# Kernel optimization log

Hardware: AMD Instinct MI355X
Metric: run time of the kernel (lower is better)

## Reference

```python
import jax, jax.numpy as jnp
import numpy as np

DIM = 128
HEADS = 8
DIM_HEAD = 128  # must equal DIM for the module's shapes to be consistent
INNER = HEADS * DIM_HEAD  # 1024
B, N = 16, 2048
SCALE = 1.0 / (DIM // 2 + 1)  # 1/65


def setup_inputs() -> dict:
    key = jax.random.key(0)
    k1, k2, k3 = jax.random.split(key, 3)
    x = jax.random.normal(k1, (B, N, DIM), dtype=jnp.float32)
    w_qkv = jax.random.normal(k2, (DIM, 3 * INNER), dtype=jnp.float32) * (DIM ** -0.5)
    w_out = jax.random.normal(k3, (INNER, DIM), dtype=jnp.float32) * (INNER ** -0.5)
    b_out = jnp.zeros((DIM,), dtype=jnp.float32)
    return {"x": x, "w_qkv": w_qkv, "w_out": w_out, "b_out": b_out}


def reference(x, w_qkv, w_out, b_out):
    b, n, dim = x.shape
    qkv = x @ w_qkv                                   # [b, n, 3*inner]
    q, k, v = jnp.split(qkv, 3, axis=-1)
    # b n (h d) -> b h n d
    to_heads = lambda t: t.reshape(b, n, HEADS, DIM_HEAD).transpose(0, 2, 1, 3)
    q, k, v = to_heads(q), to_heads(k), to_heads(v)
    xq_ft = jnp.abs(jnp.fft.rfft(q * SCALE, axis=-1))  # [b, h, n, f] real
    xk_ft = jnp.abs(jnp.fft.rfft(k * SCALE, axis=-1))
    xv_ft = jnp.fft.rfft(v, axis=-1)                   # complex
    att = jnp.einsum('bhex,bhey->bhxy', xq_ft, xk_ft)  # [b, h, f, f]
    att = jax.nn.softmax(att, axis=-1)
    xqkv_ft = jnp.einsum('bhxy,bhey->bhex', att.astype(xv_ft.dtype), xv_ft)
    out = jnp.fft.irfft(xqkv_ft, n=dim, axis=-1)       # [b, h, n, dim]
    out = out.transpose(0, 2, 1, 3).reshape(b, n, HEADS * dim)  # b n (h d)
    return out @ w_out + b_out
```

## Files before the change

### kernel.cpp

```cpp
#include <hip/hip_runtime.h>
#include <hip/hip_bf16.h>
#include <math.h>

#define NB    16
#define NSEQ  2048
#define MROWS (NB*NSEQ)

typedef __attribute__((ext_vector_type(8))) short bf16x8;
typedef __attribute__((ext_vector_type(4))) float f32x4;

__device__ __forceinline__ void g2l16(const void* g, void* l) {
    __builtin_amdgcn_global_load_lds(
        (const __attribute__((address_space(1))) void*)g,
        (__attribute__((address_space(3))) void*)l, 16, 0, 0);
}

__device__ __forceinline__ ushort f2bfu(float x) {
    __hip_bfloat16 t = __float2bfloat16(x);
    return *reinterpret_cast<ushort*>(&t);
}

__global__ __launch_bounds__(256) void k_misc(const float* __restrict__ x,
                                              const float* __restrict__ wqkv,
                                              const float* __restrict__ wout,
                                              __hip_bfloat16* __restrict__ Xb,
                                              ushort* __restrict__ Wvb,
                                              ushort* __restrict__ Wqkb,
                                              ushort* __restrict__ Gcat,
                                              ushort* __restrict__ Fcs,
                                              ushort* __restrict__ Bas) {
    __shared__ float tc[128], ts[128];
    int tid = threadIdx.x;
    int bid = blockIdx.x;
    if (bid < 4096) {
        int i = bid * 256 + tid;
        float4 v = ((const float4*)x)[i];
        __hip_bfloat16 o[4] = {__float2bfloat16(v.x), __float2bfloat16(v.y),
                               __float2bfloat16(v.z), __float2bfloat16(v.w)};
        *(ushort4*)((ushort*)Xb + (size_t)i * 4) = *(const ushort4*)o;
    } else if (bid < 4224) {
        int u = bid - 4096;
        float4 v = *(const float4*)(wqkv + (size_t)u * 3072 + 2048 + tid * 4);
        ushort o[4] = {f2bfu(v.x), f2bfu(v.y), f2bfu(v.z), f2bfu(v.w)};
        *(ushort4*)(Wvb + (size_t)u * 1024 + tid * 4) = *(const ushort4*)o;
    } else if (bid < 4352) {
        int u = bid - 4224;
        #pragma unroll
        for (int it = 0; it < 2; ++it) {
            int i = it * 256 + tid;
            float4 v = ((const float4*)(wqkv + (size_t)u * 3072))[i];
            ushort o[4] = {f2bfu(v.x), f2bfu(v.y), f2bfu(v.z), f2bfu(v.w)};
            *(ushort4*)(Wqkb + (size_t)u * 2048 + i * 4) = *(const ushort4*)o;
        }
    } else if (bid < 4872) {
        int hx = bid - 4352;
        if (tid < 128) {
            float a = (float)tid / 64.0f;
            tc[tid] = cospif(a);
            ts[tid] = sinpif(a);
        }
        __syncthreads();
        if (tid < 128) {
            int h = hx / 65, xx = hx - h * 65;
            float w = (xx == 0 || xx == 64) ? (1.0f / 128.0f) : (2.0f / 128.0f);
            float ar = 0.f, ai = 0.f;
            #pragma unroll 8
            for (int d = 0; d < 128; ++d) {
                float wv = wout[(size_t)(h * 128 + d) * 128 + tid];
                int m = (xx * d) & 127;
                ar = fmaf(wv, tc[m], ar);
                ai = fmaf(wv, ts[m], ai);
            }
            ushort* gp = Gcat + ((size_t)(h * 128 + tid)) * 160;
            gp[xx] = f2bfu(ar * w);
            gp[80 + xx] = f2bfu(-ai * w);
            if (xx == 0) {
                for (int k = 65; k < 80; ++k) gp[k] = 0;
                for (int k = 145; k < 160; ++k) gp[k] = 0;
            }
        }
    } else if (bid < 4888) {
        int r = (bid - 4872) * 16 + (tid >> 4);
        int d = r & 127;
        int y0 = (tid & 15) * 6;
        #pragma unroll
        for (int k = 0; k < 6; ++k) {
            int y = y0 + k;
            float v = 0.f;
            if (y < 65) {
                float a = (float)((d * y) & 127) / 64.0f;
                v = (r < 128) ? cospif(a) : -sinpif(a);
            }
            Fcs[r * 96 + y] = f2bfu(v);
        }
    } else {
        int idx = bid - 4888;
        int rj = idx * 16 + (tid >> 4);
        int ri = (rj >= 80) ? 1 : 0;
        int f = rj - ri * 80;
        int d0 = (tid & 15) * 8;
        #pragma unroll
        for (int k = 0; k < 8; ++k) {
            int d = d0 + k;
            float a = (float)((f * d) & 127) / 64.0f;
            float v = (ri ? -sinpif(a) : cospif(a)) * (1.0f / 65.0f);
            Bas[rj * 128 + d] = f2bfu(v);
        }
    }
}

__global__ __launch_bounds__(256) void k_wfold(const ushort* __restrict__ Wqkb,
                                               const ushort* __restrict__ Bas,
                                               ushort* __restrict__ Wt2) {
    __shared__ ushort As[64 * 128];
    __shared__ ushort Bs[160 * 128];
    int tid = threadIdx.x;
    int wave = tid >> 6, lane = tid & 63;
    int reg = blockIdx.x >> 4;
    int h = (blockIdx.x >> 1) & 7;
    int uh = blockIdx.x & 1;
    const ushort* ga = Wqkb + (size_t)(uh * 64) * 2048 + reg * 1024 + h * 128;
    #pragma unroll
    for (int it = 0; it < 4; ++it) {
        int q0 = wave * 256 + it * 64;
        int q = q0 + lane;
        int row = q >> 4, cp = q & 15;
        int gc = cp ^ (row & 15);
        g2l16(ga + (size_t)row * 2048 + gc * 8, As + q0 * 8);
    }
    #pragma unroll
    for (int it = 0; it < 10; ++it) {
        int q0 = it * 256 + wave * 64;
        int q = q0 + lane;
        int row = q >> 4, cp = q & 15;
        int gc = cp ^ (row & 15);
        g2l16(Bas + (size_t)row * 128 + gc * 8, Bs + q0 * 8);
    }
    __syncthreads();

    f32x4 acc[2][5];
    #pragma unroll
    for (int i = 0; i < 2; ++i)
        #pragma unroll
        for (int j = 0; j < 5; ++j) acc[i][j] = (f32x4){0.f, 0.f, 0.f, 0.f};

    int lr = lane & 15, lk = lane >> 4;
    int wr = (wave >> 1) * 32;
    int wn = (wave & 1) * 80;
    #pragma unroll
    for (int kk = 0; kk < 4; ++kk) {
        bf16x8 af[2], bfr[5];
        int c = kk * 4 + lk;
        #pragma unroll
        for (int i = 0; i < 2; ++i) {
            int m = wr + i * 16 + lr;
            af[i] = *(const bf16x8*)(As + m * 128 + (c ^ (m & 15)) * 8);
        }
        #pragma unroll
        for (int j = 0; j < 5; ++j) {
            int n = wn + j * 16 + lr;
            bfr[j] = *(const bf16x8*)(Bs + n * 128 + (c ^ (n & 15)) * 8);
        }
        #pragma unroll
        for (int i = 0; i < 2; ++i)
            #pragma unroll
            for (int j = 0; j < 5; ++j)
                acc[i][j] = __builtin_amdgcn_mfma_f32_16x16x32_bf16(af[i], bfr[j], acc[i][j], 0, 0, 0);
    }

    #pragma unroll
    for (int j = 0; j < 5; ++j) {
        int rj = wn + j * 16 + lr;
        int n = (h * 2 + reg) * 160 + rj;
        #pragma unroll
        for (int i = 0; i < 2; ++i) {
            int c0 = uh * 64 + wr + i * 16 + lk * 4;
            union { ushort4 u4; ushort u[4]; } pk;
            #pragma unroll
            for (int r = 0; r < 4; ++r) pk.u[r] = f2bfu(acc[i][j][r]);
            *(ushort4*)(Wt2 + (size_t)n * 128 + c0) = pk.u4;
        }
    }
}

__global__ __launch_bounds__(320, 3) void k_fuse(const __hip_bfloat16* __restrict__ Xb,
                                                 const ushort* __restrict__ Wt2,
                                                 float* __restrict__ attp) {
    __shared__ ushort As[128 * 128];
    __shared__ ushort S[160 * 128];
    int tid = threadIdx.x;
    int wave = tid >> 6, lane = tid & 63;
    int lr = lane & 15, lk = lane >> 4;
    int lin = blockIdx.y * 128 + blockIdx.x;
    int nl = (lin & 7) * 64 + (lin >> 3);
    int b = nl >> 5;
    int epart = (nl >> 3) & 3, h = nl & 7;
    size_t erow0 = (size_t)b * NSEQ + (size_t)epart * 512;
    const ushort* wh = Wt2 + (size_t)h * 320 * 128;

    bf16x8 bw[4][4];
    #pragma unroll
    for (int ks = 0; ks < 4; ++ks)
        #pragma unroll
        for (int rb = 0; rb < 4; ++rb) {
            int n = rb * 80 + wave * 16 + lr;
            bw[ks][rb] = *(const bf16x8*)(wh + (size_t)n * 128 + (ks * 4 + lk) * 8);
        }

    {
        const ushort* gx = (const ushort*)Xb + erow0 * 128;
        for (int r = wave; r < 32; r += 5) {
            int q0 = r * 64, q = q0 + lane;
            int row = q >> 4, cp = q & 15;
            int gc = cp ^ (row & 15);
            g2l16(gx + (size_t)row * 128 + gc * 8, As + q0 * 8);
        }
    }
    __syncthreads();

    f32x4 acc2[5];
    #pragma unroll
    for (int j = 0; j < 5; ++j) acc2[j] = (f32x4){0.f, 0.f, 0.f, 0.f};

    for (int it = 0; it < 4; ++it) {
        #pragma unroll
        for (int et = 0; et < 8; ++et) {
            f32x4 a4[4];
            #pragma unroll
            for (int rb = 0; rb < 4; ++rb) a4[rb] = (f32x4){0.f, 0.f, 0.f, 0.f};
            #pragma unroll
            for (int ks = 0; ks < 4; ++ks) {
                int m = et * 16 + lr;
                bf16x8 xa = *(const bf16x8*)(As + m * 128 + (((ks * 4 + lk) ^ (m & 15))) * 8);
                #pragma unroll
                for (int rb = 0; rb < 4; ++rb)
                    a4[rb] = __builtin_amdgcn_mfma_f32_16x16x32_bf16(xa, bw[ks][rb], a4[rb], 0, 0, 0);
            }
            int e4 = et * 16 + lk * 4;
            int cq = e4 >> 3, sub = e4 & 7;
            union { ushort4 u4; ushort u[4]; } pq, pk2;
            #pragma unroll
            for (int r = 0; r < 4; ++r) {
                pq.u[r]  = f2bfu(__builtin_amdgcn_sqrtf(a4[0][r] * a4[0][r] + a4[1][r] * a4[1][r]));
                pk2.u[r] = f2bfu(__builtin_amdgcn_sqrtf(a4[2][r] * a4[2][r] + a4[3][r] * a4[3][r]));
            }
            int fq = wave * 16 + lr;
            int fk = 80 + wave * 16 + lr;
            *(ushort4*)(S + fq * 128 + ((cq ^ (fq & 15)) << 3) + sub) = pq.u4;
            *(ushort4*)(S + fk * 128 + ((cq ^ (fk & 15)) << 3) + sub) = pk2.u4;
        }
        __syncthreads();
        if (it < 3) {
            const ushort* gx = (const ushort*)Xb + (erow0 + (size_t)(it + 1) * 128) * 128;
            for (int r = wave; r < 32; r += 5) {
                int q0 = r * 64, q = q0 + lane;
                int row = q >> 4, cp = q & 15;
                int gc = cp ^ (row & 15);
                g2l16(gx + (size_t)row * 128 + gc * 8, As + q0 * 8);
            }
        }
        #pragma unroll
        for (int ks = 0; ks < 4; ++ks) {
            int cg = ks * 4 + lk;
            int xr = wave * 16 + lr;
            bf16x8 qa = *(const bf16x8*)(S + xr * 128 + ((cg ^ (xr & 15)) << 3));
            #pragma unroll
            for (int kt = 0; kt < 5; ++kt) {
                int yr = 80 + kt * 16 + lr;
                bf16x8 kb = *(const bf16x8*)(S + yr * 128 + ((cg ^ (yr & 15)) << 3));
                acc2[kt] = __builtin_amdgcn_mfma_f32_16x16x32_bf16(qa, kb, acc2[kt], 0, 0, 0);
            }
        }
        __syncthreads();
    }

    float* outp = attp + ((size_t)(b * 8 + h) * 4 + epart) * 6400;
    #pragma unroll
    for (int kt = 0; kt < 5; ++kt)
        #pragma unroll
        for (int r = 0; r < 4; ++r)
            outp[(wave * 16 + lk * 4 + r) * 80 + kt * 16 + lr] = acc2[kt][r];
}

__global__ __launch_bounds__(256) void k_TP(const float* __restrict__ attp,
                                            const ushort* __restrict__ Fcs,
                                            const ushort* __restrict__ Gcat,
                                            ushort* __restrict__ Pt) {
    __shared__ ushort A3[128 * 168];
    __shared__ ushort Ab[80 * 104];
    int tid = threadIdx.x;
    int wave = tid >> 6, lane = tid & 63;
    int lr = lane & 15, quad = lane >> 4;
    int bh = blockIdx.x, chalf = blockIdx.y;
    int b = bh >> 3, h = bh & 7;

    uint2 z2; z2.x = 0; z2.y = 0;
    uint2* A3v = (uint2*)A3;
    #pragma unroll 4
    for (int i = tid; i < 128 * 168 / 4; i += 256) A3v[i] = z2;
    uint2* Abv = (uint2*)Ab;
    #pragma unroll 4
    for (int i = tid; i < 80 * 104 / 4; i += 256) Abv[i] = z2;
    __syncthreads();

    const float* pbase = attp + (size_t)bh * 4 * 6400;
    for (int p = 0; p < 17; ++p) {
        int xx = p * 4 + wave;
        if (xx < 65) {
            float v0 = 0.f, v1 = 0.f;
            #pragma unroll
            for (int c = 0; c < 4; ++c) {
                v0 += pbase[(size_t)c * 6400 + xx * 80 + lane];
                if (lane == 0) v1 += pbase[(size_t)c * 6400 + xx * 80 + 64];
            }
            float v1b = __shfl(v1, 0);
            float m = fmaxf(v0, v1b);
            #pragma unroll
            for (int off = 32; off >= 1; off >>= 1) m = fmaxf(m, __shfl_xor(m, off));
            float e0 = expf(v0 - m);
            float e1 = expf(v1b - m);
            float s = e0;
            #pragma unroll
            for (int off = 32; off >= 1; off >>= 1) s += __shfl_xor(s, off);
            s += e1;
            float inv = 1.0f / s;
            Ab[xx * 104 + lane] = f2bfu(e0 * inv);
            if (lane == 0) Ab[xx * 104 + 64] = f2bfu(e1 * inv);
        }
    }
    __syncthreads();

    f32x4 acc1[4][5];
    #pragma unroll
    for (int i = 0; i < 4; ++i)
        #pragma unroll
        for (int j = 0; j < 5; ++j) acc1[i][j] = (f32x4){0.f, 0.f, 0.f, 0.f};
    #pragma unroll
    for (int ks = 0; ks < 3; ++ks) {
        bf16x8 af[4], bfr[5];
        #pragma unroll
        for (int mi = 0; mi < 4; ++mi)
            af[mi] = *(const bf16x8*)(Fcs + (size_t)((wave * 4 + mi) * 16 + lr) * 96 + ks * 32 + quad * 8);
        #pragma unroll
        for (int nt = 0; nt < 5; ++nt)
            bfr[nt] = *(const bf16x8*)(Ab + (nt * 16 + lr) * 104 + ks * 32 + quad * 8);
        #pragma unroll
        for (int mi = 0; mi < 4; ++mi)
            #pragma unroll
            for (int nt = 0; nt < 5; ++nt)
                acc1[mi][nt] = __builtin_amdgcn_mfma_f32_16x16x32_bf16(af[mi], bfr[nt], acc1[mi][nt], 0, 0, 0);
    }
    #pragma unroll
    for (int nt = 0; nt < 5; ++nt) {
        int x = nt * 16 + lr;
        if (x < 65) {
            #pragma unroll
            for (int mi = 0; mi < 4; ++mi) {
                int wbase = (wave * 4 + mi) * 16 + quad * 4;
                #pragma unroll
                for (int r = 0; r < 4; ++r) {
                    int which = wbase + r;
                    int d = which & 127;
                    int kc = (which >> 7) * 80 + x;
                    A3[d * 168 + kc] = f2bfu(acc1[mi][nt][r]);
                }
            }
        }
    }
    __syncthreads();

    f32x4 acc2[2][4];
    #pragma unroll
    for (int i = 0; i < 2; ++i)
        #pragma unroll
        for (int j = 0; j < 4; ++j) acc2[i][j] = (f32x4){0.f, 0.f, 0.f, 0.f};
    const ushort* Gh = Gcat + (size_t)h * 128 * 160;
    #pragma unroll
    for (int ks = 0; ks < 5; ++ks) {
        bf16x8 a2[2], b2[4];
        #pragma unroll
        for (int mi = 0; mi < 2; ++mi)
            a2[mi] = *(const bf16x8*)(A3 + ((wave * 2 + mi) * 16 + lr) * 168 + ks * 32 + quad * 8);
        #pragma unroll
        for (int nt = 0; nt < 4; ++nt)
            b2[nt] = *(const bf16x8*)(Gh + (size_t)(chalf * 64 + nt * 16 + lr) * 160 + ks * 32 + quad * 8);
        #pragma unroll
        for (int mi = 0; mi < 2; ++mi)
            #pragma unroll
            for (int nt = 0; nt < 4; ++nt)
                acc2[mi][nt] = __builtin_amdgcn_mfma_f32_16x16x32_bf16(a2[mi], b2[nt], acc2[mi][nt], 0, 0, 0);
    }
    #pragma unroll
    for (int mi = 0; mi < 2; ++mi) {
        int dbase = (wave * 2 + mi) * 16 + quad * 4;
        #pragma unroll
        for (int nt = 0; nt < 4; ++nt) {
            int c = chalf * 64 + nt * 16 + lr;
            union { ushort4 u4; ushort u[4]; } pk;
            #pragma unroll
            for (int r = 0; r < 4; ++r) pk.u[r] = f2bfu(acc2[mi][nt][r]);
            *(ushort4*)(Pt + ((size_t)(b * 128 + c)) * 1024 + h * 128 + dbase) = pk.u4;
        }
    }
}

__global__ __launch_bounds__(256) void k_R(const ushort* __restrict__ Wvb,
                                           const ushort* __restrict__ Pt,
                                           ushort* __restrict__ Rt) {
    __shared__ ushort As[64 * 128];
    __shared__ ushort Bs[64 * 128];
    int tid = threadIdx.x;
    int wave = tid >> 6, lane = tid & 63;
    int b = blockIdx.x >> 2;
    int nq = (blockIdx.x >> 1) & 1;
    int uq = blockIdx.x & 1;
    const ushort* pb = Pt + (size_t)b * 128 * 1024;

    f32x4 acc[2][2];
    #pragma unroll
    for (int i = 0; i < 2; ++i)
        #pragma unroll
        for (int j = 0; j < 2; ++j) acc[i][j] = (f32x4){0.f, 0.f, 0.f, 0.f};

    int lr = lane & 15, lk = lane >> 4;
    int wr = (wave >> 1) * 32, wc = (wave & 1) * 32;

    for (int k0 = 0; k0 < 1024; k0 += 128) {
        __syncthreads();
        #pragma unroll
        for (int it = 0; it < 4; ++it) {
            int q = wave * 256 + it * 64 + lane;
            int row = q >> 4, cp = q & 15;
            int gc = cp ^ (row & 15);
            int lbase = (wave * 256 + it * 64) * 8;
            g2l16(Wvb + (size_t)(uq * 64 + row) * 1024 + k0 + gc * 8, As + lbase);
            g2l16(pb + (size_t)(nq * 64 + row) * 1024 + k0 + gc * 8, Bs + lbase);
        }
        __syncthreads();
        #pragma unroll
        for (int kk = 0; kk < 4; ++kk) {
            bf16x8 af[2], bfr[2];
            int c = kk * 4 + lk;
            #pragma unroll
            for (int i = 0; i < 2; ++i) {
                int m = wr + i * 16 + lr;
                af[i] = *(const bf16x8*)(As + m * 128 + (c ^ (m & 15)) * 8);
                int n = wc + i * 16 + lr;
                bfr[i] = *(const bf16x8*)(Bs + n * 128 + (c ^ (n & 15)) * 8);
            }
            #pragma unroll
            for (int i = 0; i < 2; ++i)
                #pragma unroll
                for (int j = 0; j < 2; ++j)
                    acc[i][j] = __builtin_amdgcn_mfma_f32_16x16x32_bf16(af[i], bfr[j], acc[i][j], 0, 0, 0);
        }
    }
    #pragma unroll
    for (int i = 0; i < 2; ++i) {
        int ubase = uq * 64 + wr + i * 16 + lk * 4;
        #pragma unroll
        for (int j = 0; j < 2; ++j) {
            int n = nq * 64 + wc + j * 16 + lr;
            union { ushort4 u4; ushort u[4]; } pk;
            #pragma unroll
            for (int r = 0; r < 4; ++r) pk.u[r] = f2bfu(acc[i][j][r]);
            *(ushort4*)(Rt + (size_t)b * 16384 + n * 128 + ubase) = pk.u4;
        }
    }
}

__global__ __launch_bounds__(256) void k_out(const __hip_bfloat16* __restrict__ Xb,
                                             const ushort* __restrict__ Rt,
                                             const float* __restrict__ bout,
                                             float* __restrict__ out) {
    __shared__ ushort As[128 * 128];
    __shared__ ushort Bs[128 * 128];
    int tid = threadIdx.x;
    int wave = tid >> 6, lane = tid & 63;
    int m0 = blockIdx.x * 128;
    int b = blockIdx.x >> 4;
    const ushort* ga = (const ushort*)Xb + (size_t)m0 * 128;
    const ushort* gb = Rt + (size_t)b * 16384;
    #pragma unroll
    for (int it = 0; it < 8; ++it) {
        int q = wave * 512 + it * 64 + lane;
        int row = q >> 4, cp = q & 15;
        int gc = cp ^ (row & 15);
        int lbase = (wave * 512 + it * 64) * 8;
        g2l16(ga + (size_t)row * 128 + gc * 8, As + lbase);
        g2l16(gb + (size_t)row * 128 + gc * 8, Bs + lbase);
    }
    __syncthreads();

    f32x4 acc[4][4];
    #pragma unroll
    for (int i = 0; i < 4; ++i)
        #pragma unroll
        for (int j = 0; j < 4; ++j) acc[i][j] = (f32x4){0.f, 0.f, 0.f, 0.f};

    int lr = lane & 15, lk = lane >> 4;
    int wr = (wave >> 1) * 64, wc = (wave & 1) * 64;
    #pragma unroll
    for (int kk = 0; kk < 4; ++kk) {
        bf16x8 af[4], bfr[4];
        int c = kk * 4 + lk;
        #pragma unroll
        for (int i = 0; i < 4; ++i) {
            int m = wr + i * 16 + lr;
            af[i] = *(const bf16x8*)(As + m * 128 + (c ^ (m & 15)) * 8);
            int n = wc + i * 16 + lr;
            bfr[i] = *(const bf16x8*)(Bs + n * 128 + (c ^ (n & 15)) * 8);
        }
        #pragma unroll
        for (int i = 0; i < 4; ++i)
            #pragma unroll
            for (int j = 0; j < 4; ++j)
                acc[i][j] = __builtin_amdgcn_mfma_f32_16x16x32_bf16(af[i], bfr[j], acc[i][j], 0, 0, 0);
    }

    #pragma unroll
    for (int i = 0; i < 4; ++i) {
        int gr = m0 + wr + i * 16 + lk * 4;
        #pragma unroll
        for (int j = 0; j < 4; ++j) {
            int gcol = wc + j * 16 + lr;
            float bias = bout[gcol];
            #pragma unroll
            for (int r = 0; r < 4; ++r)
                out[(size_t)(gr + r) * 128 + gcol] = acc[i][j][r] + bias;
        }
    }
}

extern "C" void kernel_launch(void* const* d_in, const int* in_sizes, int n_in,
                              void* d_out, int out_size, void* d_ws, size_t ws_size,
                              hipStream_t stream) {
    const float* x    = (const float*)d_in[0];
    const float* wqkv = (const float*)d_in[1];
    const float* wout = (const float*)d_in[2];
    const float* bout = (const float*)d_in[3];
    float* out = (float*)d_out;

    char* ws = (char*)d_ws;
    size_t off = 0;
    auto alloc = [&](size_t bytes) -> void* {
        void* p = (void*)(ws + off);
        off += (bytes + 255) & ~(size_t)255;
        return p;
    };
    ushort* Wt2  = (ushort*)alloc((size_t)8 * 320 * 128 * 2);
    ushort* Gcat = (ushort*)alloc((size_t)8 * 128 * 160 * 2);
    ushort* Fcs  = (ushort*)alloc((size_t)256 * 96 * 2);
    ushort* Wvb  = (ushort*)alloc((size_t)128 * 1024 * 2);
    ushort* Wqkb = (ushort*)alloc((size_t)128 * 2048 * 2);
    ushort* Bas  = (ushort*)alloc((size_t)160 * 128 * 2);
    __hip_bfloat16* Xb = (__hip_bfloat16*)alloc((size_t)MROWS * 128 * 2);
    float* attp = (float*)alloc((size_t)128 * 4 * 6400 * 4);
    ushort* Pt  = (ushort*)alloc((size_t)16 * 128 * 1024 * 2);
    ushort* Rt  = (ushort*)alloc((size_t)16 * 128 * 128 * 2);

    k_misc<<<dim3(4898), 256, 0, stream>>>(x, wqkv, wout, Xb, Wvb, Wqkb, Gcat, Fcs, Bas);
    k_wfold<<<dim3(32), 256, 0, stream>>>(Wqkb, Bas, Wt2);
    k_fuse<<<dim3(128, 4), 320, 0, stream>>>(Xb, Wt2, attp);
    k_TP<<<dim3(128, 2), 256, 0, stream>>>(attp, Fcs, Gcat, Pt);
    k_R<<<dim3(64), 256, 0, stream>>>(Wvb, Pt, Rt);
    k_out<<<dim3(256), 256, 0, stream>>>(Xb, Rt, bout, out);
}
```

Measured before the change: 168.1 us.

## Halve k_fuse tiles for higher occupancy and split softmax into its own kernel

k_fuse now processes 256-row sequence chunks with 64-row tiles instead of 512/128. It streams Wt2 fragments per half instead of holding all of them in registers, and the launch-bounds occupancy hint rises from 3 to 5 blocks. This cuts LDS and register use and doubles the grid to raise occupancy. The softmax that k_TP used to compute redundantly in each of its two blocks per head now runs once in a separate kernel that writes bf16 attention. That adds a launch and doubles the partial-sum traffic, and the Wt2 loads now repeat every iteration.

Measured after the change: 183.1 us. 1.09x slower.

```diff
diff --git a/kernel.cpp b/kernel.cpp
--- a/kernel.cpp
+++ b/kernel.cpp
@@ -183,33 +183,25 @@
     }
 }
 
-__global__ __launch_bounds__(320, 3) void k_fuse(const __hip_bfloat16* __restrict__ Xb,
+__global__ __launch_bounds__(320, 5) void k_fuse(const __hip_bfloat16* __restrict__ Xb,
                                                  const ushort* __restrict__ Wt2,
                                                  float* __restrict__ attp) {
-    __shared__ ushort As[128 * 128];
-    __shared__ ushort S[160 * 128];
+    __shared__ ushort As[64 * 128];
+    __shared__ ushort S[160 * 64];
     int tid = threadIdx.x;
     int wave = tid >> 6, lane = tid & 63;
     int lr = lane & 15, lk = lane >> 4;
     int lin = blockIdx.y * 128 + blockIdx.x;
-    int nl = (lin & 7) * 64 + (lin >> 3);
-    int b = nl >> 5;
-    int epart = (nl >> 3) & 3, h = nl & 7;
-    size_t erow0 = (size_t)b * NSEQ + (size_t)epart * 512;
+    int nl = (lin & 7) * 128 + (lin >> 3);
+    int b = nl >> 6;
+    int rem = nl & 63;
+    int h = rem >> 3, epart = rem & 7;
+    size_t erow0 = (size_t)b * NSEQ + (size_t)epart * 256;
     const ushort* wh = Wt2 + (size_t)h * 320 * 128;
-
-    bf16x8 bw[4][4];
-    #pragma unroll
-    for (int ks = 0; ks < 4; ++ks)
-        #pragma unroll
-        for (int rb = 0; rb < 4; ++rb) {
-            int n = rb * 80 + wave * 16 + lr;
-            bw[ks][rb] = *(const bf16x8*)(wh + (size_t)n * 128 + (ks * 4 + lk) * 8);
-        }
 
     {
         const ushort* gx = (const ushort*)Xb + erow0 * 128;
-        for (int r = wave; r < 32; r += 5) {
+        for (int r = wave; r < 16; r += 5) {
             int q0 = r * 64, q = q0 + lane;
             int row = q >> 4, cp = q & 15;
             int gc = cp ^ (row & 15);
@@ -224,35 +216,41 @@
 
     for (int it = 0; it < 4; ++it) {
         #pragma unroll
-        for (int et = 0; et < 8; ++et) {
-            f32x4 a4[4];
-            #pragma unroll
-            for (int rb = 0; rb < 4; ++rb) a4[rb] = (f32x4){0.f, 0.f, 0.f, 0.f};
-            #pragma unroll
-            for (int ks = 0; ks < 4; ++ks) {
-                int m = et * 16 + lr;
-                bf16x8 xa = *(const bf16x8*)(As + m * 128 + (((ks * 4 + lk) ^ (m & 15))) * 8);
+        for (int p = 0; p < 2; ++p) {
+            bf16x8 bwp[4][2];
+            #pragma unroll
+            for (int ks = 0; ks < 4; ++ks)
                 #pragma unroll
-                for (int rb = 0; rb < 4; ++rb)
-                    a4[rb] = __builtin_amdgcn_mfma_f32_16x16x32_bf16(xa, bw[ks][rb], a4[rb], 0, 0, 0);
-            }
-            int e4 = et * 16 + lk * 4;
-            int cq = e4 >> 3, sub = e4 & 7;
-            union { ushort4 u4; ushort u[4]; } pq, pk2;
-            #pragma unroll
-            for (int r = 0; r < 4; ++r) {
-                pq.u[r]  = f2bfu(__builtin_amdgcn_sqrtf(a4[0][r] * a4[0][r] + a4[1][r] * a4[1][r]));
-                pk2.u[r] = f2bfu(__builtin_amdgcn_sqrtf(a4[2][r] * a4[2][r] + a4[3][r] * a4[3][r]));
-            }
-            int fq = wave * 16 + lr;
-            int fk = 80 + wave * 16 + lr;
-            *(ushort4*)(S + fq * 128 + ((cq ^ (fq & 15)) << 3) + sub) = pq.u4;
-            *(ushort4*)(S + fk * 128 + ((cq ^ (fk & 15)) << 3) + sub) = pk2.u4;
+                for (int j = 0; j < 2; ++j) {
+                    int n = (p * 2 + j) * 80 + wave * 16 + lr;
+                    bwp[ks][j] = *(const bf16x8*)(wh + (size_t)n * 128 + (ks * 4 + lk) * 8);
+                }
+            #pragma unroll
+            for (int et = 0; et < 4; ++et) {
+                f32x4 a2[2];
+                a2[0] = (f32x4){0.f, 0.f, 0.f, 0.f};
+                a2[1] = (f32x4){0.f, 0.f, 0.f, 0.f};
+                #pragma unroll
+                for (int ks = 0; ks < 4; ++ks) {
+                    int m = et * 16 + lr;
+                    bf16x8 xa = *(const bf16x8*)(As + m * 128 + (((ks * 4 + lk) ^ (m & 15))) * 8);
+                    a2[0] = __builtin_amdgcn_mfma_f32_16x16x32_bf16(xa, bwp[ks][0], a2[0], 0, 0, 0);
+                    a2[1] = __builtin_amdgcn_mfma_f32_16x16x32_bf16(xa, bwp[ks][1], a2[1], 0, 0, 0);
+                }
+                int e4 = et * 16 + lk * 4;
+                int cq = e4 >> 3, sub = e4 & 7;
+                union { ushort4 u4; ushort u[4]; } pm;
+                #pragma unroll
+                for (int r = 0; r < 4; ++r)
+                    pm.u[r] = f2bfu(__builtin_amdgcn_sqrtf(a2[0][r] * a2[0][r] + a2[1][r] * a2[1][r]));
+                int f = p * 80 + wave * 16 + lr;
+                *(ushort4*)(S + f * 64 + ((cq ^ (f & 7)) << 3) + sub) = pm.u4;
+            }
         }
         __syncthreads();
         if (it < 3) {
-            const ushort* gx = (const ushort*)Xb + (erow0 + (size_t)(it + 1) * 128) * 128;
-            for (int r = wave; r < 32; r += 5) {
+            const ushort* gx = (const ushort*)Xb + (erow0 + (size_t)(it + 1) * 64) * 128;
+            for (int r = wave; r < 16; r += 5) {
                 int q0 = r * 64, q = q0 + lane;
                 int row = q >> 4, cp = q & 15;
                 int gc = cp ^ (row & 15);
@@ -260,21 +258,21 @@
             }
         }
         #pragma unroll
-        for (int ks = 0; ks < 4; ++ks) {
-            int cg = ks * 4 + lk;
+        for (int ksq = 0; ksq < 2; ++ksq) {
+            int cg = ksq * 4 + lk;
             int xr = wave * 16 + lr;
-            bf16x8 qa = *(const bf16x8*)(S + xr * 128 + ((cg ^ (xr & 15)) << 3));
+            bf16x8 qa = *(const bf16x8*)(S + xr * 64 + ((cg ^ (xr & 7)) << 3));
             #pragma unroll
             for (int kt = 0; kt < 5; ++kt) {
                 int yr = 80 + kt * 16 + lr;
-                bf16x8 kb = *(const bf16x8*)(S + yr * 128 + ((cg ^ (yr & 15)) << 3));
+                bf16x8 kb = *(const bf16x8*)(S + yr * 64 + ((cg ^ (yr & 7)) << 3));
                 acc2[kt] = __builtin_amdgcn_mfma_f32_16x16x32_bf16(qa, kb, acc2[kt], 0, 0, 0);
             }
         }
         __syncthreads();
     }
 
-    float* outp = attp + ((size_t)(b * 8 + h) * 4 + epart) * 6400;
+    float* outp = attp + ((size_t)(b * 8 + h) * 8 + epart) * 6400;
     #pragma unroll
     for (int kt = 0; kt < 5; ++kt)
         #pragma unroll
@@ -282,53 +280,56 @@
             outp[(wave * 16 + lk * 4 + r) * 80 + kt * 16 + lr] = acc2[kt][r];
 }
 
-__global__ __launch_bounds__(256) void k_TP(const float* __restrict__ attp,
+__global__ void k_softmax(const float* __restrict__ attp, ushort* __restrict__ AttB) {
+    int xx = blockIdx.x;
+    int bh = blockIdx.y;
+    int lane = threadIdx.x;
+    ushort* Ab = AttB + (size_t)bh * 8320;
+    if (xx >= 65) {
+        Ab[xx * 104 + lane] = 0;
+        if (lane < 40) Ab[xx * 104 + 64 + lane] = 0;
+        return;
+    }
+    const float* base = attp + (size_t)bh * 8 * 6400 + xx * 80;
+    float v0 = 0.f, v1 = 0.f;
+    #pragma unroll
+    for (int c = 0; c < 8; ++c) {
+        v0 += base[(size_t)c * 6400 + lane];
+        if (lane == 0) v1 += base[(size_t)c * 6400 + 64];
+    }
+    float v1b = __shfl(v1, 0);
+    float m = fmaxf(v0, v1b);
+    #pragma unroll
+    for (int off = 32; off >= 1; off >>= 1) m = fmaxf(m, __shfl_xor(m, off));
+    float e0 = expf(v0 - m);
+    float e1 = expf(v1b - m);
+    float s = e0;
+    #pragma unroll
+    for (int off = 32; off >= 1; off >>= 1) s += __shfl_xor(s, off);
+    s += e1;
+    float inv = 1.0f / s;
+    Ab[xx * 104 + lane] = f2bfu(e0 * inv);
+    if (lane == 0) Ab[xx * 104 + 64] = f2bfu(e1 * inv);
+    if (lane < 39) Ab[xx * 104 + 65 + lane] = 0;
+}
+
+__global__ __launch_bounds__(256) void k_TP(const ushort* __restrict__ AttB,
                                             const ushort* __restrict__ Fcs,
                                             const ushort* __restrict__ Gcat,
                                             ushort* __restrict__ Pt) {
     __shared__ ushort A3[128 * 168];
-    __shared__ ushort Ab[80 * 104];
     int tid = threadIdx.x;
     int wave = tid >> 6, lane = tid & 63;
     int lr = lane & 15, quad = lane >> 4;
-    int bh = blockIdx.x, chalf = blockIdx.y;
+    int chalf = blockIdx.x, bh = blockIdx.y;
     int b = bh >> 3, h = bh & 7;
 
     uint2 z2; z2.x = 0; z2.y = 0;
     uint2* A3v = (uint2*)A3;
     #pragma unroll 4
     for (int i = tid; i < 128 * 168 / 4; i += 256) A3v[i] = z2;
-    uint2* Abv = (uint2*)Ab;
-    #pragma unroll 4
-    for (int i = tid; i < 80 * 104 / 4; i += 256) Abv[i] = z2;
     __syncthreads();
-
-    const float* pbase = attp + (size_t)bh * 4 * 6400;
-    for (int p = 0; p < 17; ++p) {
-        int xx = p * 4 + wave;
-        if (xx < 65) {
-            float v0 = 0.f, v1 = 0.f;
-            #pragma unroll
-            for (int c = 0; c < 4; ++c) {
-                v0 += pbase[(size_t)c * 6400 + xx * 80 + lane];
-                if (lane == 0) v1 += pbase[(size_t)c * 6400 + xx * 80 + 64];
-            }
-            float v1b = __shfl(v1, 0);
-            float m = fmaxf(v0, v1b);
-            #pragma unroll
-            for (int off = 32; off >= 1; off >>= 1) m = fmaxf(m, __shfl_xor(m, off));
-            float e0 = expf(v0 - m);
-            float e1 = expf(v1b - m);
-            float s = e0;
-            #pragma unroll
-            for (int off = 32; off >= 1; off >>= 1) s += __shfl_xor(s, off);
-            s += e1;
-            float inv = 1.0f / s;
-            Ab[xx * 104 + lane] = f2bfu(e0 * inv);
-            if (lane == 0) Ab[xx * 104 + 64] = f2bfu(e1 * inv);
-        }
-    }
-    __syncthreads();
+    const ushort* Ab = AttB + (size_t)bh * 8320;
 
     f32x4 acc1[4][5];
     #pragma unroll
@@ -555,14 +556,16 @@
     ushort* Wqkb = (ushort*)alloc((size_t)128 * 2048 * 2);
     ushort* Bas  = (ushort*)alloc((size_t)160 * 128 * 2);
     __hip_bfloat16* Xb = (__hip_bfloat16*)alloc((size_t)MROWS * 128 * 2);
-    float* attp = (float*)alloc((size_t)128 * 4 * 6400 * 4);
+    float* attp = (float*)alloc((size_t)128 * 8 * 6400 * 4);
+    ushort* AttB = (ushort*)alloc((size_t)128 * 8320 * 2);
     ushort* Pt  = (ushort*)alloc((size_t)16 * 128 * 1024 * 2);
     ushort* Rt  = (ushort*)alloc((size_t)16 * 128 * 128 * 2);
 
     k_misc<<<dim3(4898), 256, 0, stream>>>(x, wqkv, wout, Xb, Wvb, Wqkb, Gcat, Fcs, Bas);
     k_wfold<<<dim3(32), 256, 0, stream>>>(Wqkb, Bas, Wt2);
-    k_fuse<<<dim3(128, 4), 320, 0, stream>>>(Xb, Wt2, attp);
-    k_TP<<<dim3(128, 2), 256, 0, stream>>>(attp, Fcs, Gcat, Pt);
+    k_fuse<<<dim3(128, 8), 320, 0, stream>>>(Xb, Wt2, attp);
+    k_softmax<<<dim3(80, 128), 64, 0, stream>>>(attp, AttB);
+    k_TP<<<dim3(2, 128), 256, 0, stream>>>(AttB, Fcs, Gcat, Pt);
     k_R<<<dim3(64), 256, 0, stream>>>(Wvb, Pt, Rt);
     k_out<<<dim3(256), 256, 0, stream>>>(Xb, Rt, bout, out);
 }
```
